# Kernel optimization log

Hardware: AMD Instinct MI355X
Metric: run time of the kernel (lower is better)

## Reference

```python
import jax, jax.numpy as jnp
import numpy as np
from jax import lax

B, L, H = 2, 1024, 1024
D = 2048          # intermediate_size
N = 16            # ssm state size
K = 4             # conv kernel
R = 64            # time_step_rank


def setup_inputs() -> dict:
    key = jax.random.key(0)
    ks = jax.random.split(key, 10)
    def nrm(k, shape, scale=0.02):
        return jax.random.normal(k, shape, dtype=jnp.float32) * scale
    A = jnp.arange(1, N + 1, dtype=jnp.float32)[None, :] * jnp.ones((D, 1), jnp.float32)
    return {
        "hidden_states": jax.random.normal(ks[0], (B, L, H), dtype=jnp.float32),
        "W_in":  nrm(ks[1], (2 * D, H)),
        "conv_w": nrm(ks[2], (D, 1, K), 0.1),
        "conv_b": nrm(ks[3], (D,), 0.1),
        "W_x":   nrm(ks[4], (R + 2 * N, D)),
        "W_dt":  nrm(ks[5], (D, R), 0.1),
        "b_dt":  jnp.full((D,), -4.6, jnp.float32),  # softplus(-4.6) ~ 0.01 dt init
        "A_log": jnp.log(A),
        "D_param": jnp.ones((D,), jnp.float32),
        "W_out": nrm(ks[6], (H, D)),
    }


def _mamba_forward(hidden_states, W_in, conv_w, conv_b, W_x, W_dt, b_dt, A_log, D_param, W_out):
    silu = jax.nn.silu
    # in_proj -> [B, L, 2D], chunk into x and gate
    proj = jnp.einsum("blh,eh->ble", hidden_states, W_in)
    x, gate = jnp.split(proj, 2, axis=-1)           # [B,L,D] each
    # depthwise causal conv over time: [B,D,L]
    xc = x.swapaxes(1, 2)
    xc = lax.conv_general_dilated(
        xc, conv_w, window_strides=(1,), padding=[(K - 1, 0)],
        dimension_numbers=("NCH", "OIH", "NCH"), feature_group_count=D)
    x = silu(xc + conv_b[None, :, None]).swapaxes(1, 2)   # [B,L,D]
    # x_proj -> dt, Bmat, Cmat
    ssm_p = jnp.einsum("bld,rd->blr", x, W_x)             # [B,L,R+2N]
    dt_lr, Bm, Cm = ssm_p[..., :R], ssm_p[..., R:R + N], ssm_p[..., R + N:]
    dt = jax.nn.softplus(jnp.einsum("blr,dr->bld", dt_lr, W_dt) + b_dt)  # [B,L,D]
    A = -jnp.exp(A_log)                                   # [D,N]
    dA = jnp.exp(dt[..., None] * A[None, None])           # [B,L,D,N]
    dBu = dt[..., None] * Bm[:, :, None, :] * x[..., None]  # [B,L,D,N]
    # selective scan over time
    def step(h, inp):
        dA_t, dBu_t, C_t = inp                            # [B,D,N],[B,D,N],[B,N]
        h = dA_t * h + dBu_t
        y = jnp.einsum("bdn,bn->bd", h, C_t)
        return h, y
    h0 = jnp.zeros((B, D, N), dt.dtype)
    _, ys = lax.scan(step, h0, (dA.swapaxes(0, 1), dBu.swapaxes(0, 1), Cm.swapaxes(0, 1)))
    y = ys.swapaxes(0, 1)                                 # [B,L,D]
    y = (y + x * D_param[None, None, :]) * silu(gate)
    return jnp.einsum("bld,hd->blh", y, W_out)            # [B,L,H]


def reference(hidden_states, W_in, conv_w, conv_b, W_x, W_dt, b_dt, A_log, D_param, W_out):
    return _mamba_forward(hidden_states, W_in, conv_w, conv_b, W_x, W_dt, b_dt, A_log, D_param, W_out)
```

## Files before the change

### kernel.cpp

```cpp
#include <hip/hip_runtime.h>
#include <hip/hip_bf16.h>
#include <math.h>

#define B_ 2
#define L_ 1024
#define H_ 1024
#define D_ 2048
#define N_ 16
#define R_ 64
#define NCK 32
#define CL 32

typedef short short8 __attribute__((ext_vector_type(8)));
typedef float floatx4 __attribute__((ext_vector_type(4)));

__device__ __forceinline__ float siluf(float g) {
    return g / (1.0f + __expf(-g));
}

__device__ __forceinline__ unsigned short f2bf(float f) {
    unsigned int u = __float_as_uint(f);
    u = (u + 0x7fffu + ((u >> 16) & 1u)) >> 16;
    return (unsigned short)u;
}

__device__ __forceinline__ float bf2f(unsigned short u) {
    return __uint_as_float(((unsigned int)u) << 16);
}

__device__ __forceinline__ void gl2lds(const unsigned short* g, unsigned short* l) {
    __builtin_amdgcn_global_load_lds(
        (const __attribute__((address_space(1))) unsigned int*)g,
        (__attribute__((address_space(3))) unsigned int*)l, 16, 0, 0);
}

#define Q0 524288
#define Q1 1572864
#define Q2 2097152
#define Q3 2146304
#define Q4 2179072
__global__ __launch_bounds__(256) void cvt_all(
    const float* __restrict__ i0, const float* __restrict__ i1,
    const float* __restrict__ i2, const float* __restrict__ i3,
    const float* __restrict__ i4,
    unsigned short* __restrict__ o0, unsigned short* __restrict__ o1,
    unsigned short* __restrict__ o2, unsigned short* __restrict__ o3,
    unsigned short* __restrict__ o4)
{
    int q = blockIdx.x * 256 + threadIdx.x;
    if (q >= Q4) return;
    const float* in; unsigned short* out; int base;
    if (q < Q0)      { in = i0; out = o0; base = 0; }
    else if (q < Q1) { in = i1; out = o1; base = Q0; }
    else if (q < Q2) { in = i2; out = o2; base = Q1; }
    else if (q < Q3) { in = i3; out = o3; base = Q2; }
    else             { in = i4; out = o4; base = Q3; }
    int i = (q - base) * 4;
    float4 v = *(const float4*)(in + i);
    ushort4 o;
    o.x = f2bf(v.x); o.y = f2bf(v.y); o.z = f2bf(v.z); o.w = f2bf(v.w);
    *(ushort4*)(out + i) = o;
}

template<int EPI>
__global__ __launch_bounds__(256) void gemm_bf16_nt(
    const unsigned short* __restrict__ A, const unsigned short* __restrict__ Bm,
    float* __restrict__ C, int K, int Ncols, int ldc, int kChunk, int nMax,
    size_t partStride, float* __restrict__ C2)
{
    __shared__ unsigned short As[128 * 32];
    __shared__ unsigned short Bs[128 * 32];
    const int tid  = threadIdx.x;
    const int lane = tid & 63;
    const int wave = tid >> 6;
    const int wm = (wave >> 1) * 64;
    const int wn = (wave & 1) * 64;
    const int lr   = lane & 15;
    const int quad = lane >> 4;
    const int m0 = blockIdx.y * 128;
    const int n0 = blockIdx.x * 128;
    const int k0 = blockIdx.z * kChunk;

    const int srow = wave * 32 + (lane >> 2);
    const int sq   = (lane & 3) * 8;
    unsigned short* AsB0 = &As[(wave * 32) * 32];
    unsigned short* AsB1 = &As[(wave * 32 + 16) * 32];
    unsigned short* BsB0 = &Bs[(wave * 32) * 32];
    unsigned short* BsB1 = &Bs[(wave * 32 + 16) * 32];
    const size_t aoff0 = (size_t)(m0 + srow) * K + sq;
    const size_t aoff1 = (size_t)(m0 + srow + 16) * K + sq;
    const size_t boff0 = (size_t)min(n0 + srow, nMax - 1) * K + sq;
    const size_t boff1 = (size_t)min(n0 + srow + 16, nMax - 1) * K + sq;

    floatx4 acc[4][4];
#pragma unroll
    for (int mi = 0; mi < 4; ++mi)
#pragma unroll
        for (int ni = 0; ni < 4; ++ni)
            acc[mi][ni] = (floatx4){0.f, 0.f, 0.f, 0.f};

    for (int kt = k0; kt < k0 + kChunk; kt += 32) {
        __syncthreads();
        gl2lds(A + aoff0 + kt, AsB0);
        gl2lds(A + aoff1 + kt, AsB1);
        gl2lds(Bm + boff0 + kt, BsB0);
        gl2lds(Bm + boff1 + kt, BsB1);
        __syncthreads();
        short8 af[4], bf[4];
#pragma unroll
        for (int mi = 0; mi < 4; ++mi)
            af[mi] = *(const short8*)&As[(wm + mi * 16 + lr) * 32 + quad * 8];
#pragma unroll
        for (int ni = 0; ni < 4; ++ni)
            bf[ni] = *(const short8*)&Bs[(wn + ni * 16 + lr) * 32 + quad * 8];
#pragma unroll
        for (int mi = 0; mi < 4; ++mi)
#pragma unroll
            for (int ni = 0; ni < 4; ++ni)
                acc[mi][ni] = __builtin_amdgcn_mfma_f32_16x16x32_bf16(
                    af[mi], bf[ni], acc[mi][ni], 0, 0, 0);
    }

    float* Cz = C + (size_t)blockIdx.z * partStride;
#pragma unroll
    for (int mi = 0; mi < 4; ++mi)
#pragma unroll
        for (int ni = 0; ni < 4; ++ni) {
            const int rr = m0 + wm + mi * 16 + quad * 4;
            const int cc = n0 + wn + ni * 16 + lr;
            if (cc >= Ncols) continue;
            if (EPI == 4) {
                if (n0 < 2048) {
                    float4 v = make_float4(acc[mi][ni][0], acc[mi][ni][1],
                                           acc[mi][ni][2], acc[mi][ni][3]);
                    *(float4*)&C[(size_t)cc * ldc + rr] = v;
                } else {
#pragma unroll
                    for (int r = 0; r < 4; ++r)
                        C2[(size_t)(rr + r) * 2048 + (cc - 2048)] = acc[mi][ni][r];
                }
            } else {
#pragma unroll
                for (int r = 0; r < 4; ++r)
                    Cz[(size_t)(rr + r) * ldc + cc] = acc[mi][ni][r];
            }
        }
}

__global__ __launch_bounds__(256) void reduce_ssm(
    const float* __restrict__ P, float* __restrict__ ssm_p,
    unsigned short* __restrict__ sp64)
{
    const int q = blockIdx.x * 256 + threadIdx.x;
    const int m = q / 24;
    const int c = (q - m * 24) * 4;
    const size_t idx = (size_t)m * 96 + c;
    float4 s = make_float4(0.f, 0.f, 0.f, 0.f);
#pragma unroll
    for (int z = 0; z < 16; ++z) {
        float4 v = *(const float4*)(P + (size_t)z * (2048 * 96) + idx);
        s.x += v.x; s.y += v.y; s.z += v.z; s.w += v.w;
    }
    *(float4*)(ssm_p + idx) = s;
    if (c < 64) {
        ushort4 o;
        o.x = f2bf(s.x); o.y = f2bf(s.y); o.z = f2bf(s.z); o.w = f2bf(s.w);
        *(ushort4*)(sp64 + (size_t)m * 64 + c) = o;
    }
}

__global__ __launch_bounds__(256) void reduce_out(
    const float* __restrict__ P, float* __restrict__ out)
{
    const size_t i = ((size_t)blockIdx.x * 256 + threadIdx.x) * 4;
    float4 a = *(const float4*)(P + i);
    float4 b = *(const float4*)(P + 2097152 + i);
    float4 c = *(const float4*)(P + 2 * 2097152 + i);
    float4 d = *(const float4*)(P + 3 * 2097152 + i);
    *(float4*)(out + i) = make_float4(a.x + b.x + c.x + d.x,
                                      a.y + b.y + c.y + d.y,
                                      a.z + b.z + c.z + d.z,
                                      a.w + b.w + c.w + d.w);
}

__global__ __launch_bounds__(256) void dt_gemm(
    const unsigned short* __restrict__ A,
    const unsigned short* __restrict__ Bm,
    float* __restrict__ C,
    const float* __restrict__ bias)
{
    __shared__ unsigned short As[64 * 72];
    __shared__ unsigned short Bs[64 * 72];
    const int tid = threadIdx.x;
    const int lane = tid & 63;
    const int wave = tid >> 6;
    const int lr = lane & 15;
    const int quad = lane >> 4;
    const int n0 = blockIdx.x * 64;
    const int m0 = blockIdx.y * 64;

    {
        const int row = tid >> 3;
        const int cq = (tid & 7) * 8;
        uint4 a0 = *(const uint4*)(A + (size_t)(m0 + row) * 64 + cq);
        uint4 a1 = *(const uint4*)(A + (size_t)(m0 + 32 + row) * 64 + cq);
        uint4 b0 = *(const uint4*)(Bm + (size_t)(n0 + row) * 64 + cq);
        uint4 b1 = *(const uint4*)(Bm + (size_t)(n0 + 32 + row) * 64 + cq);
        *(uint4*)&As[row * 72 + cq] = a0;
        *(uint4*)&As[(32 + row) * 72 + cq] = a1;
        *(uint4*)&Bs[row * 72 + cq] = b0;
        *(uint4*)&Bs[(32 + row) * 72 + cq] = b1;
    }
    __syncthreads();

    floatx4 acc[4];
#pragma unroll
    for (int ni = 0; ni < 4; ++ni) acc[ni] = (floatx4){0.f, 0.f, 0.f, 0.f};

#pragma unroll
    for (int kt = 0; kt < 64; kt += 32) {
        short8 af = *(const short8*)&As[(wave * 16 + lr) * 72 + kt + quad * 8];
#pragma unroll
        for (int ni = 0; ni < 4; ++ni) {
            short8 bf = *(const short8*)&Bs[(ni * 16 + lr) * 72 + kt + quad * 8];
            acc[ni] = __builtin_amdgcn_mfma_f32_16x16x32_bf16(af, bf, acc[ni], 0, 0, 0);
        }
    }

    const int rr = m0 + wave * 16 + quad * 4;
#pragma unroll
    for (int ni = 0; ni < 4; ++ni) {
        const int cc = n0 + ni * 16 + lr;
        const float bv = bias[cc];
#pragma unroll
        for (int r = 0; r < 4; ++r) {
            const float z = acc[ni][r] + bv;
            const float spv = fmaxf(z, 0.f) + __logf(1.f + __expf(-fabsf(z)));
            C[(size_t)(rr + r) * 2048 + cc] = spv;
        }
    }
}

__global__ __launch_bounds__(256) void conv_silu_kernel(
    const float* __restrict__ projx, const float* __restrict__ conv_w,
    const float* __restrict__ conv_b, unsigned short* __restrict__ x_bf)
{
    __shared__ unsigned short tile[64][72];
    const int t = threadIdx.x;
    const int d0 = blockIdx.x * 64;
    const int lt0 = blockIdx.y * 64;
    const int b = blockIdx.z;
    const int dl = t & 63;
    const int seg = t >> 6;
    const int d = d0 + dl;
    const int l0 = lt0 + seg * 16;
    const float* row = projx + (size_t)d * 2048 + b * 1024;
    const float w0 = conv_w[d * 4 + 0], w1 = conv_w[d * 4 + 1];
    const float w2 = conv_w[d * 4 + 2], w3 = conv_w[d * 4 + 3];
    const float bias = conv_b[d];

    float p[19];
    p[0] = (l0 >= 3) ? row[l0 - 3] : 0.f;
    p[1] = (l0 >= 2) ? row[l0 - 2] : 0.f;
    p[2] = (l0 >= 1) ? row[l0 - 1] : 0.f;
#pragma unroll
    for (int j = 0; j < 16; j += 4) {
        float4 q = *(const float4*)(row + l0 + j);
        p[3 + j] = q.x; p[4 + j] = q.y; p[5 + j] = q.z; p[6 + j] = q.w;
    }
#pragma unroll
    for (int j = 0; j < 16; ++j) {
        float v = siluf(bias + w0 * p[j] + w1 * p[j + 1] + w2 * p[j + 2] + w3 * p[j + 3]);
        tile[seg * 16 + j][dl] = f2bf(v);
    }
    __syncthreads();

    const int ml = t >> 2;
    const int c = t & 3;
    short8 s0 = *(const short8*)&tile[ml][c * 16];
    short8 s1 = *(const short8*)&tile[ml][c * 16 + 8];
    unsigned short* dst = x_bf + (size_t)(b * 1024 + lt0 + ml) * 2048 + d0 + c * 16;
    *(short8*)dst = s0;
    *(short8*)(dst + 8) = s1;
}

__global__ __launch_bounds__(256) void scan_p1(
    const float* __restrict__ dt, const unsigned short* __restrict__ x_bf,
    const float* __restrict__ sp, const float* __restrict__ A_log,
    float* __restrict__ Pch, float* __restrict__ Hch)
{
    __shared__ float sB[CL][16];
    const int tid = threadIdx.x;
    const int d = blockIdx.x * 256 + tid;
    const int ck = blockIdx.y;
    const int b = blockIdx.z;
    const int mb = b * 1024 + ck * CL;

    if (tid < CL * 4) {
        int row = tid >> 2, q = (tid & 3) * 4;
        *(float4*)&sB[row][q] = *(const float4*)(sp + (size_t)(mb + row) * 96 + 64 + q);
    }
    float An2[16];
    {
        const float* al = A_log + d * 16;
#pragma unroll
        for (int j = 0; j < 16; j += 4) {
            float4 a4 = *(const float4*)(al + j);
            An2[j + 0] = -__expf(a4.x) * 1.44269504f;
            An2[j + 1] = -__expf(a4.y) * 1.44269504f;
            An2[j + 2] = -__expf(a4.z) * 1.44269504f;
            An2[j + 3] = -__expf(a4.w) * 1.44269504f;
        }
    }
    __syncthreads();

    float h[16];
#pragma unroll
    for (int n = 0; n < 16; ++n) h[n] = 0.f;
    float dts = 0.f;

    for (int l = 0; l < CL; ++l) {
        const size_t off = (size_t)(mb + l) * 2048 + d;
        const float dtv = dt[off];
        const float xv = bf2f(x_bf[off]);
        const float u = dtv * xv;
        dts += dtv;
        float4 B0 = *(const float4*)&sB[l][0];
        float4 B1 = *(const float4*)&sB[l][4];
        float4 B2 = *(const float4*)&sB[l][8];
        float4 B3 = *(const float4*)&sB[l][12];
        float Bv[16] = {B0.x, B0.y, B0.z, B0.w, B1.x, B1.y, B1.z, B1.w,
                        B2.x, B2.y, B2.z, B2.w, B3.x, B3.y, B3.z, B3.w};
#pragma unroll
        for (int n = 0; n < 16; ++n) {
            const float dA = __builtin_amdgcn_exp2f(dtv * An2[n]);
            h[n] = fmaf(dA, h[n], Bv[n] * u);
        }
    }

    const size_t base = ((size_t)(b * NCK + ck) * 2048 + d) * 16;
#pragma unroll
    for (int j = 0; j < 16; j += 4) {
        float4 pv = make_float4(__builtin_amdgcn_exp2f(dts * An2[j]),
                                __builtin_amdgcn_exp2f(dts * An2[j + 1]),
                                __builtin_amdgcn_exp2f(dts * An2[j + 2]),
                                __builtin_amdgcn_exp2f(dts * An2[j + 3]));
        *(float4*)(Pch + base + j) = pv;
        *(float4*)(Hch + base + j) = make_float4(h[j], h[j + 1], h[j + 2], h[j + 3]);
    }
}

__global__ __launch_bounds__(256) void scan_combine(
    float* __restrict__ Pch, const float* __restrict__ Hch)
{
    const int flat = blockIdx.x * 256 + threadIdx.x;
    const int dn = flat & 32767;
    const int b = flat >> 15;
    float hin = 0.f;
#pragma unroll 4
    for (int ck = 0; ck < NCK; ++ck) {
        const size_t a = ((size_t)(b * NCK + ck) << 15) + dn;
        const float p = Pch[a];
        const float hc = Hch[a];
        Pch[a] = hin;
        hin = fmaf(p, hin, hc);
    }
}

__global__ __launch_bounds__(256) void scan_p2(
    const float* __restrict__ dt, const unsigned short* __restrict__ x_bf,
    const float* __restrict__ gate, const float* __restrict__ sp,
    const float* __restrict__ A_log, const float* __restrict__ Dp,
    const float* __restrict__ Hin, unsigned short* __restrict__ y_bf)
{
    __shared__ float sBC[CL][32];
    const int tid = threadIdx.x;
    const int d = blockIdx.x * 256 + tid;
    const int ck = blockIdx.y;
    const int b = blockIdx.z;
    const int mb = b * 1024 + ck * CL;

    {
        int row = tid >> 3, q = (tid & 7) * 4;
        *(float4*)&sBC[row][q] = *(const float4*)(sp + (size_t)(mb + row) * 96 + 64 + q);
    }
    float An2[16];
    {
        const float* al = A_log + d * 16;
#pragma unroll
        for (int j = 0; j < 16; j += 4) {
            float4 a4 = *(const float4*)(al + j);
            An2[j + 0] = -__expf(a4.x) * 1.44269504f;
            An2[j + 1] = -__expf(a4.y) * 1.44269504f;
            An2[j + 2] = -__expf(a4.z) * 1.44269504f;
            An2[j + 3] = -__expf(a4.w) * 1.44269504f;
        }
    }
    float h[16];
    {
        const size_t base = ((size_t)(b * NCK + ck) * 2048 + d) * 16;
#pragma unroll
        for (int j = 0; j < 16; j += 4) {
            float4 hv = *(const float4*)(Hin + base + j);
            h[j] = hv.x; h[j + 1] = hv.y; h[j + 2] = hv.z; h[j + 3] = hv.w;
        }
    }
    const float Dv = Dp[d];
    __syncthreads();

    for (int l = 0; l < CL; ++l) {
        const size_t off = (size_t)(mb + l) * 2048 + d;
        const float dtv = dt[off];
        const float xv = bf2f(x_bf[off]);
        const float gv = gate[off];
        const float u = dtv * xv;
        float4 B0 = *(const float4*)&sBC[l][0];
        float4 B1 = *(const float4*)&sBC[l][4];
        float4 B2 = *(const float4*)&sBC[l][8];
        float4 B3 = *(const float4*)&sBC[l][12];
        float Bv[16] = {B0.x, B0.y, B0.z, B0.w, B1.x, B1.y, B1.z, B1.w,
                        B2.x, B2.y, B2.z, B2.w, B3.x, B3.y, B3.z, B3.w};
#pragma unroll
        for (int n = 0; n < 16; ++n) {
            const float dA = __builtin_amdgcn_exp2f(dtv * An2[n]);
            h[n] = fmaf(dA, h[n], Bv[n] * u);
        }
        float4 C0 = *(const float4*)&sBC[l][16];
        float4 C1 = *(const float4*)&sBC[l][20];
        float4 C2 = *(const float4*)&sBC[l][24];
        float4 C3 = *(const float4*)&sBC[l][28];
        float Cv[16] = {C0.x, C0.y, C0.z, C0.w, C1.x, C1.y, C1.z, C1.w,
                        C2.x, C2.y, C2.z, C2.w, C3.x, C3.y, C3.z, C3.w};
        float p = 0.f;
#pragma unroll
        for (int n = 0; n < 16; ++n)
            p = fmaf(h[n], Cv[n], p);
        y_bf[off] = f2bf(fmaf(xv, Dv, p) * siluf(gv));
    }
}

extern "C" void kernel_launch(void* const* d_in, const int* in_sizes, int n_in,
                              void* d_out, int out_size, void* d_ws, size_t ws_size,
                              hipStream_t stream)
{
    const float* hs     = (const float*)d_in[0];
    const float* W_in   = (const float*)d_in[1];
    const float* conv_w = (const float*)d_in[2];
    const float* conv_b = (const float*)d_in[3];
    const float* W_x    = (const float*)d_in[4];
    const float* W_dt   = (const float*)d_in[5];
    const float* b_dt   = (const float*)d_in[6];
    const float* A_log  = (const float*)d_in[7];
    const float* Dp     = (const float*)d_in[8];
    const float* W_out  = (const float*)d_in[9];
    float* out = (float*)d_out;

    float* ws    = (float*)d_ws;
    float* gate  = ws;
    float* dtb   = gate + (size_t)4194304;
    float* projx = dtb + (size_t)4194304;
    float* ssm_p = projx + (size_t)4194304;
    unsigned short* hs_bf    = (unsigned short*)(ssm_p + 196608);
    unsigned short* W_in_bf  = hs_bf + (size_t)2097152;
    unsigned short* W_out_bf = W_in_bf + (size_t)4194304;
    unsigned short* W_x_bf   = W_out_bf + (size_t)2097152;
    unsigned short* W_dt_bf  = W_x_bf + (size_t)196608;
    unsigned short* sp64_bf  = W_dt_bf + (size_t)131072;
    unsigned short* x_bf     = sp64_bf + (size_t)131072;
    float* P1   = projx;
    float* Pch  = projx;
    float* Hch  = projx + (size_t)2097152;
    float* Pout = gate;
    unsigned short* y_bf = hs_bf;

    const int M = B_ * L_;

    cvt_all<<<(Q4 + 255) / 256, 256, 0, stream>>>(
        hs, W_in, W_out, W_x, W_dt, hs_bf, W_in_bf, W_out_bf, W_x_bf, W_dt_bf);

    gemm_bf16_nt<4><<<dim3(4096 / 128, M / 128, 1), 256, 0, stream>>>(
        hs_bf, W_in_bf, projx, 1024, 4096, 2048, 1024, 4096, 0, gate);

    conv_silu_kernel<<<dim3(D_ / 64, L_ / 64, B_), 256, 0, stream>>>(
        projx, conv_w, conv_b, x_bf);

    gemm_bf16_nt<0><<<dim3(1, M / 128, 16), 256, 0, stream>>>(
        x_bf, W_x_bf, P1, 2048, 96, 96, 128, 96, (size_t)2048 * 96, nullptr);

    reduce_ssm<<<(2048 * 24) / 256, 256, 0, stream>>>(P1, ssm_p, sp64_bf);

    dt_gemm<<<dim3(2048 / 64, 2048 / 64), 256, 0, stream>>>(
        sp64_bf, W_dt_bf, dtb, b_dt);

    scan_p1<<<dim3(D_ / 256, NCK, B_), 256, 0, stream>>>(
        dtb, x_bf, ssm_p, A_log, Pch, Hch);
    scan_combine<<<(B_ * D_ * 16) / 256, 256, 0, stream>>>(Pch, Hch);
    scan_p2<<<dim3(D_ / 256, NCK, B_), 256, 0, stream>>>(
        dtb, x_bf, gate, ssm_p, A_log, Dp, Pch, y_bf);

    gemm_bf16_nt<0><<<dim3(1024 / 128, M / 128, 4), 256, 0, stream>>>(
        y_bf, W_out_bf, Pout, 2048, 1024, 1024, 512, 1024, (size_t)2048 * 1024, nullptr);

    reduce_out<<<(2048 * 1024 / 4) / 256, 256, 0, stream>>>(Pout, out);
}
```

Measured before the change: 236.0 us.

## Replace split-K out-projection with direct GEMM and store per-chunk dt sums

The out-projection no longer runs as a 4-way split-K GEMM followed by a reduction kernel. A dedicated 128x64-tile double-buffered bf16 MFMA GEMM writes the final output directly, which removes the partial-sum traffic and one launch. The scan's first pass now stores only the per-chunk dt sum rather than 16 decay products per state. The combine kernel recomputes the decays with exp2, cutting writes and reads. In exchange the output GEMM launches only 256 blocks over the full K=2048, so it has less parallelism than the split-K version.

```diff
diff --git a/kernel.cpp b/kernel.cpp
--- a/kernel.cpp
+++ b/kernel.cpp
@@ -147,6 +147,80 @@
         }
 }
 
+__global__ __launch_bounds__(256) void gemm_out(
+    const unsigned short* __restrict__ A,
+    const unsigned short* __restrict__ Bm,
+    float* __restrict__ C)
+{
+    __shared__ unsigned short As[2][128 * 32];
+    __shared__ unsigned short Bs[2][64 * 32];
+    const int tid  = threadIdx.x;
+    const int lane = tid & 63;
+    const int wave = tid >> 6;
+    const int wm = (wave >> 1) * 64;
+    const int wn = (wave & 1) * 32;
+    const int lr   = lane & 15;
+    const int quad = lane >> 4;
+    const int m0 = blockIdx.y * 128;
+    const int n0 = blockIdx.x * 64;
+
+    const int arow = wave * 32 + (lane >> 2);
+    const int brow = wave * 16 + (lane >> 2);
+    const int sq   = (lane & 3) * 8;
+    const size_t aoff0 = (size_t)(m0 + arow) * 2048 + sq;
+    const size_t aoff1 = (size_t)(m0 + arow + 16) * 2048 + sq;
+    const size_t boff  = (size_t)(n0 + brow) * 2048 + sq;
+
+    floatx4 acc[4][2];
+#pragma unroll
+    for (int mi = 0; mi < 4; ++mi)
+#pragma unroll
+        for (int ni = 0; ni < 2; ++ni)
+            acc[mi][ni] = (floatx4){0.f, 0.f, 0.f, 0.f};
+
+    gl2lds(A + aoff0, &As[0][(wave * 32) * 32]);
+    gl2lds(A + aoff1, &As[0][(wave * 32 + 16) * 32]);
+    gl2lds(Bm + boff, &Bs[0][(wave * 16) * 32]);
+    __syncthreads();
+
+    int cur = 0;
+    for (int t = 0; t < 64; ++t) {
+        if (t < 63) {
+            const int nx = cur ^ 1;
+            const int kt = (t + 1) * 32;
+            gl2lds(A + aoff0 + kt, &As[nx][(wave * 32) * 32]);
+            gl2lds(A + aoff1 + kt, &As[nx][(wave * 32 + 16) * 32]);
+            gl2lds(Bm + boff + kt, &Bs[nx][(wave * 16) * 32]);
+        }
+        short8 af[4], bf[2];
+#pragma unroll
+        for (int mi = 0; mi < 4; ++mi)
+            af[mi] = *(const short8*)&As[cur][(wm + mi * 16 + lr) * 32 + quad * 8];
+#pragma unroll
+        for (int ni = 0; ni < 2; ++ni)
+            bf[ni] = *(const short8*)&Bs[cur][(wn + ni * 16 + lr) * 32 + quad * 8];
+#pragma unroll
+        for (int mi = 0; mi < 4; ++mi)
+#pragma unroll
+            for (int ni = 0; ni < 2; ++ni)
+                acc[mi][ni] = __builtin_amdgcn_mfma_f32_16x16x32_bf16(
+                    af[mi], bf[ni], acc[mi][ni], 0, 0, 0);
+        __syncthreads();
+        cur ^= 1;
+    }
+
+#pragma unroll
+    for (int mi = 0; mi < 4; ++mi)
+#pragma unroll
+        for (int ni = 0; ni < 2; ++ni) {
+            const int rr = m0 + wm + mi * 16 + quad * 4;
+            const int cc = n0 + wn + ni * 16 + lr;
+#pragma unroll
+            for (int r = 0; r < 4; ++r)
+                C[(size_t)(rr + r) * 1024 + cc] = acc[mi][ni][r];
+        }
+}
+
 __global__ __launch_bounds__(256) void reduce_ssm(
     const float* __restrict__ P, float* __restrict__ ssm_p,
     unsigned short* __restrict__ sp64)
@@ -167,20 +241,6 @@
         o.x = f2bf(s.x); o.y = f2bf(s.y); o.z = f2bf(s.z); o.w = f2bf(s.w);
         *(ushort4*)(sp64 + (size_t)m * 64 + c) = o;
     }
-}
-
-__global__ __launch_bounds__(256) void reduce_out(
-    const float* __restrict__ P, float* __restrict__ out)
-{
-    const size_t i = ((size_t)blockIdx.x * 256 + threadIdx.x) * 4;
-    float4 a = *(const float4*)(P + i);
-    float4 b = *(const float4*)(P + 2097152 + i);
-    float4 c = *(const float4*)(P + 2 * 2097152 + i);
-    float4 d = *(const float4*)(P + 3 * 2097152 + i);
-    *(float4*)(out + i) = make_float4(a.x + b.x + c.x + d.x,
-                                      a.y + b.y + c.y + d.y,
-                                      a.z + b.z + c.z + d.z,
-                                      a.w + b.w + c.w + d.w);
 }
 
 __global__ __launch_bounds__(256) void dt_gemm(
@@ -287,7 +347,7 @@
 __global__ __launch_bounds__(256) void scan_p1(
     const float* __restrict__ dt, const unsigned short* __restrict__ x_bf,
     const float* __restrict__ sp, const float* __restrict__ A_log,
-    float* __restrict__ Pch, float* __restrict__ Hch)
+    float* __restrict__ Dts, float* __restrict__ Hch)
 {
     __shared__ float sB[CL][16];
     const int tid = threadIdx.x;
@@ -338,31 +398,31 @@
         }
     }
 
-    const size_t base = ((size_t)(b * NCK + ck) * 2048 + d) * 16;
-#pragma unroll
-    for (int j = 0; j < 16; j += 4) {
-        float4 pv = make_float4(__builtin_amdgcn_exp2f(dts * An2[j]),
-                                __builtin_amdgcn_exp2f(dts * An2[j + 1]),
-                                __builtin_amdgcn_exp2f(dts * An2[j + 2]),
-                                __builtin_amdgcn_exp2f(dts * An2[j + 3]));
-        *(float4*)(Pch + base + j) = pv;
+    const size_t cb = (size_t)(b * NCK + ck) * 2048 + d;
+    Dts[cb] = dts;
+    const size_t base = cb * 16;
+#pragma unroll
+    for (int j = 0; j < 16; j += 4)
         *(float4*)(Hch + base + j) = make_float4(h[j], h[j + 1], h[j + 2], h[j + 3]);
-    }
 }
 
 __global__ __launch_bounds__(256) void scan_combine(
-    float* __restrict__ Pch, const float* __restrict__ Hch)
+    const float* __restrict__ Dts, const float* __restrict__ Hch,
+    const float* __restrict__ A_log, float* __restrict__ Hin)
 {
     const int flat = blockIdx.x * 256 + threadIdx.x;
     const int dn = flat & 32767;
     const int b = flat >> 15;
+    const int d = dn >> 4;
+    const float An2 = -__expf(A_log[dn]) * 1.44269504f;
     float hin = 0.f;
 #pragma unroll 4
     for (int ck = 0; ck < NCK; ++ck) {
+        const size_t cb = (size_t)(b * NCK + ck) * 2048 + d;
+        const float p = __builtin_amdgcn_exp2f(Dts[cb] * An2);
         const size_t a = ((size_t)(b * NCK + ck) << 15) + dn;
-        const float p = Pch[a];
         const float hc = Hch[a];
-        Pch[a] = hin;
+        Hin[a] = hin;
         hin = fmaf(p, hin, hc);
     }
 }
@@ -467,10 +527,10 @@
     unsigned short* W_dt_bf  = W_x_bf + (size_t)196608;
     unsigned short* sp64_bf  = W_dt_bf + (size_t)131072;
     unsigned short* x_bf     = sp64_bf + (size_t)131072;
+    float* Dts  = (float*)(x_bf + (size_t)4194304);
     float* P1   = projx;
-    float* Pch  = projx;
+    float* Hin  = projx;
     float* Hch  = projx + (size_t)2097152;
-    float* Pout = gate;
     unsigned short* y_bf = hs_bf;
 
     const int M = B_ * L_;
@@ -493,13 +553,10 @@
         sp64_bf, W_dt_bf, dtb, b_dt);
 
     scan_p1<<<dim3(D_ / 256, NCK, B_), 256, 0, stream>>>(
-        dtb, x_bf, ssm_p, A_log, Pch, Hch);
-    scan_combine<<<(B_ * D_ * 16) / 256, 256, 0, stream>>>(Pch, Hch);
+        dtb, x_bf, ssm_p, A_log, Dts, Hch);
+    scan_combine<<<(B_ * D_ * 16) / 256, 256, 0, stream>>>(Dts, Hch, A_log, Hin);
     scan_p2<<<dim3(D_ / 256, NCK, B_), 256, 0, stream>>>(
-        dtb, x_bf, gate, ssm_p, A_log, Dp, Pch, y_bf);
-
-    gemm_bf16_nt<0><<<dim3(1024 / 128, M / 128, 4), 256, 0, stream>>>(
-        y_bf, W_out_bf, Pout, 2048, 1024, 1024, 512, 1024, (size_t)2048 * 1024, nullptr);
-
-    reduce_out<<<(2048 * 1024 / 4) / 256, 256, 0, stream>>>(Pout, out);
-}
+        dtb, x_bf, gate, ssm_p, A_log, Dp, Hin, y_bf);
+
+    gemm_out<<<dim3(1024 / 64, M / 128), 256, 0, stream>>>(y_bf, W_out_bf, out);
+}
```

New measurement: 246.9 us. 1.05x slower.

## Store in_proj x row-major, transpose in conv via LDS, pass per-chunk dt sums

Applied to the files above, without the earlier changes.

The in_proj GEMM epilogue now writes the x half row-major with scalar stores instead of transposed float4 stores. The conv kernel stages a 67x64 tile through shared memory so it can read along time. Separately, scan_p1 now stores one dt-sum per (chunk,d) instead of 16 decay products. scan_combine recomputes the decay with exp2 from A_log, cutting the intermediate traffic and splitting the chunk-state buffer into Hch and Hin. This trades transposed global writes for an LDS transpose and adds some recomputation in the combine step.

```diff
diff --git a/kernel.cpp b/kernel.cpp
--- a/kernel.cpp
+++ b/kernel.cpp
@@ -130,10 +130,10 @@
             const int cc = n0 + wn + ni * 16 + lr;
             if (cc >= Ncols) continue;
             if (EPI == 4) {
-                if (n0 < 2048) {
-                    float4 v = make_float4(acc[mi][ni][0], acc[mi][ni][1],
-                                           acc[mi][ni][2], acc[mi][ni][3]);
-                    *(float4*)&C[(size_t)cc * ldc + rr] = v;
+                if (cc < 2048) {
+#pragma unroll
+                    for (int r = 0; r < 4; ++r)
+                        C[(size_t)(rr + r) * 2048 + cc] = acc[mi][ni][r];
                 } else {
 #pragma unroll
                     for (int r = 0; r < 4; ++r)
@@ -242,32 +242,55 @@
 }
 
 __global__ __launch_bounds__(256) void conv_silu_kernel(
-    const float* __restrict__ projx, const float* __restrict__ conv_w,
+    const float* __restrict__ xpre, const float* __restrict__ conv_w,
     const float* __restrict__ conv_b, unsigned short* __restrict__ x_bf)
 {
+    __shared__ float inT[67][64];
     __shared__ unsigned short tile[64][72];
     const int t = threadIdx.x;
     const int d0 = blockIdx.x * 64;
     const int lt0 = blockIdx.y * 64;
     const int b = blockIdx.z;
+
+    {
+        const int r = t >> 2;
+        const int q = (t & 3) * 16;
+        const int l = lt0 + r - 3;
+        if (l >= 0) {
+            const float* src = xpre + ((size_t)(b * 1024 + l)) * 2048 + d0 + q;
+            *(float4*)&inT[r][q + 0]  = *(const float4*)(src + 0);
+            *(float4*)&inT[r][q + 4]  = *(const float4*)(src + 4);
+            *(float4*)&inT[r][q + 8]  = *(const float4*)(src + 8);
+            *(float4*)&inT[r][q + 12] = *(const float4*)(src + 12);
+        } else {
+            float4 z4 = make_float4(0.f, 0.f, 0.f, 0.f);
+            *(float4*)&inT[r][q + 0]  = z4;
+            *(float4*)&inT[r][q + 4]  = z4;
+            *(float4*)&inT[r][q + 8]  = z4;
+            *(float4*)&inT[r][q + 12] = z4;
+        }
+        if (t < 12) {
+            const int r2 = 64 + (t >> 2);
+            const int l2 = lt0 + r2 - 3;
+            const float* src = xpre + ((size_t)(b * 1024 + l2)) * 2048 + d0 + q;
+            *(float4*)&inT[r2][q + 0]  = *(const float4*)(src + 0);
+            *(float4*)&inT[r2][q + 4]  = *(const float4*)(src + 4);
+            *(float4*)&inT[r2][q + 8]  = *(const float4*)(src + 8);
+            *(float4*)&inT[r2][q + 12] = *(const float4*)(src + 12);
+        }
+    }
+    __syncthreads();
+
     const int dl = t & 63;
     const int seg = t >> 6;
     const int d = d0 + dl;
-    const int l0 = lt0 + seg * 16;
-    const float* row = projx + (size_t)d * 2048 + b * 1024;
     const float w0 = conv_w[d * 4 + 0], w1 = conv_w[d * 4 + 1];
     const float w2 = conv_w[d * 4 + 2], w3 = conv_w[d * 4 + 3];
     const float bias = conv_b[d];
 
     float p[19];
-    p[0] = (l0 >= 3) ? row[l0 - 3] : 0.f;
-    p[1] = (l0 >= 2) ? row[l0 - 2] : 0.f;
-    p[2] = (l0 >= 1) ? row[l0 - 1] : 0.f;
-#pragma unroll
-    for (int j = 0; j < 16; j += 4) {
-        float4 q = *(const float4*)(row + l0 + j);
-        p[3 + j] = q.x; p[4 + j] = q.y; p[5 + j] = q.z; p[6 + j] = q.w;
-    }
+#pragma unroll
+    for (int j = 0; j < 19; ++j) p[j] = inT[seg * 16 + j][dl];
 #pragma unroll
     for (int j = 0; j < 16; ++j) {
         float v = siluf(bias + w0 * p[j] + w1 * p[j + 1] + w2 * p[j + 2] + w3 * p[j + 3]);
@@ -287,7 +310,7 @@
 __global__ __launch_bounds__(256) void scan_p1(
     const float* __restrict__ dt, const unsigned short* __restrict__ x_bf,
     const float* __restrict__ sp, const float* __restrict__ A_log,
-    float* __restrict__ Pch, float* __restrict__ Hch)
+    float* __restrict__ Dts, float* __restrict__ Hch)
 {
     __shared__ float sB[CL][16];
     const int tid = threadIdx.x;
@@ -338,31 +361,31 @@
         }
     }
 
-    const size_t base = ((size_t)(b * NCK + ck) * 2048 + d) * 16;
-#pragma unroll
-    for (int j = 0; j < 16; j += 4) {
-        float4 pv = make_float4(__builtin_amdgcn_exp2f(dts * An2[j]),
-                                __builtin_amdgcn_exp2f(dts * An2[j + 1]),
-                                __builtin_amdgcn_exp2f(dts * An2[j + 2]),
-                                __builtin_amdgcn_exp2f(dts * An2[j + 3]));
-        *(float4*)(Pch + base + j) = pv;
+    const size_t cb = (size_t)(b * NCK + ck) * 2048 + d;
+    Dts[cb] = dts;
+    const size_t base = cb * 16;
+#pragma unroll
+    for (int j = 0; j < 16; j += 4)
         *(float4*)(Hch + base + j) = make_float4(h[j], h[j + 1], h[j + 2], h[j + 3]);
-    }
 }
 
 __global__ __launch_bounds__(256) void scan_combine(
-    float* __restrict__ Pch, const float* __restrict__ Hch)
+    const float* __restrict__ Dts, const float* __restrict__ Hch,
+    const float* __restrict__ A_log, float* __restrict__ Hin)
 {
     const int flat = blockIdx.x * 256 + threadIdx.x;
     const int dn = flat & 32767;
     const int b = flat >> 15;
+    const int d = dn >> 4;
+    const float An2 = -__expf(A_log[dn]) * 1.44269504f;
     float hin = 0.f;
 #pragma unroll 4
     for (int ck = 0; ck < NCK; ++ck) {
+        const size_t cb = (size_t)(b * NCK + ck) * 2048 + d;
+        const float p = __builtin_amdgcn_exp2f(Dts[cb] * An2);
         const size_t a = ((size_t)(b * NCK + ck) << 15) + dn;
-        const float p = Pch[a];
         const float hc = Hch[a];
-        Pch[a] = hin;
+        Hin[a] = hin;
         hin = fmaf(p, hin, hc);
     }
 }
@@ -458,8 +481,8 @@
     float* ws    = (float*)d_ws;
     float* gate  = ws;
     float* dtb   = gate + (size_t)4194304;
-    float* projx = dtb + (size_t)4194304;
-    float* ssm_p = projx + (size_t)4194304;
+    float* xpre  = dtb + (size_t)4194304;
+    float* ssm_p = xpre + (size_t)4194304;
     unsigned short* hs_bf    = (unsigned short*)(ssm_p + 196608);
     unsigned short* W_in_bf  = hs_bf + (size_t)2097152;
     unsigned short* W_out_bf = W_in_bf + (size_t)4194304;
@@ -467,9 +490,10 @@
     unsigned short* W_dt_bf  = W_x_bf + (size_t)196608;
     unsigned short* sp64_bf  = W_dt_bf + (size_t)131072;
     unsigned short* x_bf     = sp64_bf + (size_t)131072;
-    float* P1   = projx;
-    float* Pch  = projx;
-    float* Hch  = projx + (size_t)2097152;
+    float* Dts  = (float*)(x_bf + (size_t)4194304);
+    float* P1   = xpre;
+    float* Hin  = xpre;
+    float* Hch  = xpre + (size_t)2097152;
     float* Pout = gate;
     unsigned short* y_bf = hs_bf;
 
@@ -479,10 +503,10 @@
         hs, W_in, W_out, W_x, W_dt, hs_bf, W_in_bf, W_out_bf, W_x_bf, W_dt_bf);
 
     gemm_bf16_nt<4><<<dim3(4096 / 128, M / 128, 1), 256, 0, stream>>>(
-        hs_bf, W_in_bf, projx, 1024, 4096, 2048, 1024, 4096, 0, gate);
+        hs_bf, W_in_bf, xpre, 1024, 4096, 2048, 1024, 4096, 0, gate);
 
     conv_silu_kernel<<<dim3(D_ / 64, L_ / 64, B_), 256, 0, stream>>>(
-        projx, conv_w, conv_b, x_bf);
+        xpre, conv_w, conv_b, x_bf);
 
     gemm_bf16_nt<0><<<dim3(1, M / 128, 16), 256, 0, stream>>>(
         x_bf, W_x_bf, P1, 2048, 96, 96, 128, 96, (size_t)2048 * 96, nullptr);
@@ -493,10 +517,10 @@
         sp64_bf, W_dt_bf, dtb, b_dt);
 
     scan_p1<<<dim3(D_ / 256, NCK, B_), 256, 0, stream>>>(
-        dtb, x_bf, ssm_p, A_log, Pch, Hch);
-    scan_combine<<<(B_ * D_ * 16) / 256, 256, 0, stream>>>(Pch, Hch);
+        dtb, x_bf, ssm_p, A_log, Dts, Hch);
+    scan_combine<<<(B_ * D_ * 16) / 256, 256, 0, stream>>>(Dts, Hch, A_log, Hin);
     scan_p2<<<dim3(D_ / 256, NCK, B_), 256, 0, stream>>>(
-        dtb, x_bf, gate, ssm_p, A_log, Dp, Pch, y_bf);
+        dtb, x_bf, gate, ssm_p, A_log, Dp, Hin, y_bf);
 
     gemm_bf16_nt<0><<<dim3(1024 / 128, M / 128, 4), 256, 0, stream>>>(
         y_bf, W_out_bf, Pout, 2048, 1024, 1024, 512, 1024, (size_t)2048 * 1024, nullptr);
```

Measured after the change: 234.3 us. About the same (-0.7%).
